# Kernel optimization log

Measured on AMD Instinct MI355X. Metric: run time of the kernel, lower is better.

The kernel has to match this reference:

```python
import jax, jax.numpy as jnp
import numpy as np

NUM_CLASSES = [5, 7, 4, 6, 3, 8, 5, 4, 6, 7, 3, 5, 4, 6, 8, 5, 7, 4, 6, 3]
N_ONE_HOTS = 20
N_OTHERS = 30
H = 48
W = 48
B = 128
N_MAP = 32
ENC_OUT = 32
RES_C = 128
OH_EMB = 9
SUM_NC = sum(NUM_CLASSES)  # 106


def conv2d(x, w, b=None, pad=0):
    # x: NCHW, w: OIHW
    y = jax.lax.conv_general_dilated(
        x, w, window_strides=(1, 1), padding=[(pad, pad), (pad, pad)],
        dimension_numbers=('NCHW', 'OIHW', 'NCHW'))
    if b is not None:
        y = y + b[None, :, None, None]
    return y


def setup_inputs() -> dict:
    key = jax.random.key(0)
    ks = jax.random.split(key, 20)
    x = jax.random.normal(ks[0], (B, 1 + N_MAP, H, W), dtype=jnp.float32)
    # first N_ONE_HOTS entries of flattened channel 0 are categorical indices
    idx_cols = [jax.random.randint(jax.random.fold_in(ks[1], j), (B,), 0, nc)
                for j, nc in enumerate(NUM_CLASSES)]
    idx = jnp.stack(idx_cols, axis=1).astype(jnp.float32)  # (B, 20)
    x = x.at[:, 0, 0, :N_ONE_HOTS].set(idx)
    s = 0.05
    inp = {
        'x': x,
        'fc_w': jax.random.normal(ks[2], (OH_EMB, SUM_NC), jnp.float32) * s,
        'fc_b': jnp.zeros((OH_EMB,), jnp.float32),
        'oh_conv_w': jax.random.normal(ks[3], (OH_EMB, OH_EMB, 1, 1), jnp.float32) * s,
        'oh_conv_b': jnp.zeros((OH_EMB,), jnp.float32),
        'others_conv_w': jax.random.normal(ks[4], (N_OTHERS, N_OTHERS, 1, 1), jnp.float32) * s,
        'others_conv_b': jnp.zeros((N_OTHERS,), jnp.float32),
        'all_conv_w': jax.random.normal(ks[5], (ENC_OUT, OH_EMB + N_OTHERS, 1, 1), jnp.float32) * s,
        'all_conv_b': jnp.zeros((ENC_OUT,), jnp.float32),
        'conv1_w': jax.random.normal(ks[6], (RES_C, ENC_OUT + N_MAP, 1, 1), jnp.float32) * s,
        'conv1_b': jnp.zeros((RES_C,), jnp.float32),
        'rconv1_w': jax.random.normal(ks[7], (RES_C, RES_C, 5, 5), jnp.float32) * s,
        'rconv1_b': jnp.zeros((RES_C,), jnp.float32),
        'rconv2_w': jax.random.normal(ks[8], (RES_C, RES_C, 5, 5), jnp.float32) * s,
        'rconv2_b': jnp.zeros((RES_C,), jnp.float32),
        'se_w1': jax.random.normal(ks[9], (RES_C // 16, RES_C), jnp.float32) * s,
        'se_w2': jax.random.normal(ks[10], (RES_C, RES_C // 16), jnp.float32) * s,
    }
    return inp


def reference(x, fc_w, fc_b, oh_conv_w, oh_conv_b, others_conv_w, others_conv_b,
              all_conv_w, all_conv_b, conv1_w, conv1_b, rconv1_w, rconv1_b,
              rconv2_w, rconv2_b, se_w1, se_w2):
    b = x.shape[0]
    gi = x[:, 0].reshape(b, -1)                 # (b, H*W)
    map_feature = x[:, 1:]                      # (b, N_MAP, H, W)
    idx = jax.lax.stop_gradient(gi[:, :N_ONE_HOTS]).astype(jnp.int32)
    others = gi[:, N_ONE_HOTS:N_ONE_HOTS + N_OTHERS]   # (b, 30)
    # vectorized one-hot build (replaces the quadratic python loop)
    oh = jnp.concatenate(
        [jax.nn.one_hot(idx[:, j], nc, dtype=x.dtype) for j, nc in enumerate(NUM_CLASSES)],
        axis=1)                                 # (b, SUM_NC)
    v = oh @ fc_w.T + fc_b                      # (b, 9)
    # faithful torch expand((h,w)+shape).reshape((b,-1,h,w)) semantics
    v = jnp.broadcast_to(v, (H, W, b, OH_EMB)).reshape(b, OH_EMB, H, W)
    o = jnp.broadcast_to(others, (H, W, b, N_OTHERS)).reshape(b, N_OTHERS, H, W)
    v = conv2d(v, oh_conv_w, oh_conv_b)
    o = conv2d(o, others_conv_w, others_conv_b)
    gi_map = conv2d(jnp.concatenate([v, o], axis=1), all_conv_w, all_conv_b)  # (b, 32, H, W)
    h = conv2d(jnp.concatenate([gi_map, map_feature], axis=1), conv1_w, conv1_b)  # (b, 128, H, W)
    # residual block: 5x5 convs, LeakyReLU, SE, identity skip (in==out)
    identity = h
    y = jax.nn.leaky_relu(conv2d(h, rconv1_w, rconv1_b, pad=2))
    y = conv2d(y, rconv2_w, rconv2_b, pad=2)
    s = y.mean(axis=(2, 3))                     # (b, 128)
    s = jax.nn.sigmoid(jax.nn.relu(s @ se_w1.T) @ se_w2.T)
    y = y * s[:, :, None, None]
    return jax.nn.leaky_relu(y + identity)
```

## Files before the change

kernel.cpp:

```cpp
#include <hip/hip_runtime.h>
#include <hip/hip_bf16.h>
#include <cstddef>

#define HH 48
#define WW 48
#define PIX 2304
#define PPIX 2704
#define BB 128
#define RESC 128
#define XCH 33

typedef short bf16x8 __attribute__((ext_vector_type(8)));
typedef float f32x4 __attribute__((ext_vector_type(4)));

static __device__ __forceinline__ float b2f(unsigned short u) {
    unsigned x = ((unsigned)u) << 16;
    return __builtin_bit_cast(float, x);
}
static __device__ __forceinline__ unsigned short f2b(float f) {
    __hip_bfloat16 hb = __float2bfloat16(f);
    return __builtin_bit_cast(unsigned short, hb);
}

#define GLOAD_LDS16(gp, lp) __builtin_amdgcn_global_load_lds( \
    (const __attribute__((address_space(1))) void*)(gp), \
    (__attribute__((address_space(3))) void*)(lp), 16, 0, 0)

__global__ void k_compute_v(const float* __restrict__ x, const float* __restrict__ fc_w,
                            const float* __restrict__ fc_b, float* __restrict__ v) {
    int b = blockIdx.x * blockDim.x + threadIdx.x;
    if (b >= BB) return;
    const int off[20] = {0,5,12,16,22,25,33,38,42,48,55,58,63,67,73,81,86,93,97,103};
    const float* gi = x + (size_t)b * XCH * PIX;
    int cols[20];
    #pragma unroll
    for (int j = 0; j < 20; j++) cols[j] = off[j] + (int)gi[j];
    #pragma unroll
    for (int e = 0; e < 9; e++) {
        float acc = fc_b[e];
        #pragma unroll
        for (int j = 0; j < 20; j++) acc += fc_w[e * 106 + cols[j]];
        v[b * 9 + e] = acc;
    }
}

__global__ void k_compute_G(const float* __restrict__ x, const float* __restrict__ v,
                            const float* __restrict__ ohw, const float* __restrict__ ohb,
                            const float* __restrict__ otw, const float* __restrict__ otb,
                            const float* __restrict__ aw,  const float* __restrict__ ab,
                            const float* __restrict__ c1w, const float* __restrict__ c1b,
                            float* __restrict__ G) {
    int p = blockIdx.x * blockDim.x + threadIdx.x;
    if (p >= PIX) return;
    float sv = v[((p / 9) & 127) * 9 + (p % 9)];
    float om[30];
    #pragma unroll
    for (int c2 = 0; c2 < 30; c2++) {
        int tmp = c2 * 24 + p;
        int c = tmp % 30;
        int bb = (c2 * 76 + tmp / 30) & 127;
        om[c2] = x[(size_t)bb * XCH * PIX + 20 + c];
    }
    float v9[9];
    #pragma unroll
    for (int e = 0; e < 9; e++) {
        float srow = 0.f;
        #pragma unroll
        for (int e2 = 0; e2 < 9; e2++) srow += ohw[e * 9 + e2];
        v9[e] = ohb[e] + srow * sv;
    }
    float o30[30];
    #pragma unroll
    for (int c = 0; c < 30; c++) {
        float a = otb[c];
        #pragma unroll
        for (int c2 = 0; c2 < 30; c2++) a += otw[c * 30 + c2] * om[c2];
        o30[c] = a;
    }
    float gi32[32];
    #pragma unroll
    for (int g = 0; g < 32; g++) {
        float a = ab[g];
        #pragma unroll
        for (int e = 0; e < 9; e++) a += aw[g * 39 + e] * v9[e];
        #pragma unroll
        for (int c = 0; c < 30; c++) a += aw[g * 39 + 9 + c] * o30[c];
        gi32[g] = a;
    }
    for (int oc = 0; oc < 128; oc++) {
        float a = c1b[oc];
        #pragma unroll
        for (int g = 0; g < 32; g++) a += c1w[oc * 64 + g] * gi32[g];
        G[p * 128 + oc] = a;
    }
}

__global__ void k_convert_w(const float* __restrict__ w1, const float* __restrict__ w2,
                            __hip_bfloat16* __restrict__ wb1, __hip_bfloat16* __restrict__ wb2) {
    int i = blockIdx.x * 256 + threadIdx.x;
    if (i >= 25 * 128 * 128) return;
    int tap = i / 16384, r = i % 16384;
    int oc = r >> 7, ic = r & 127;
    size_t src = (size_t)(oc * 128 + ic) * 25 + tap;
    wb1[i] = __float2bfloat16(w1[src]);
    wb2[i] = __float2bfloat16(w2[src]);
}

__global__ void k_zero_border(__hip_bfloat16* __restrict__ a, __hip_bfloat16* __restrict__ b2) {
    int img = blockIdx.x, t = threadIdx.x;
    for (int j = t; j < 6400; j += 256) {
        int pb = j >> 4, c16 = j & 15;
        int y, x2;
        if (pb < 208) { int q = pb / 52; y = q < 2 ? q : q + 48; x2 = pb % 52; }
        else { int r = pb - 208; y = 2 + (r >> 2); int c = r & 3; x2 = c < 2 ? c : c + 48; }
        size_t off = ((size_t)img * PPIX + y * 52 + x2) * 128 + c16 * 8;
        uint4 z = {0, 0, 0, 0};
        *(uint4*)(a + off) = z;
        *(uint4*)(b2 + off) = z;
    }
}

__global__ __launch_bounds__(256) void k_conv1(const float* __restrict__ x, const float* __restrict__ c1w,
                                               const float* __restrict__ G, __hip_bfloat16* __restrict__ h) {
    __shared__ float xm[32][64];
    __shared__ float w1[32][128];
    int b = blockIdx.y, p0 = blockIdx.x * 64;
    int t = threadIdx.x;
    for (int i = t; i < 4096; i += 256) { int m = i >> 7, oc = i & 127; w1[m][oc] = c1w[oc * 64 + 32 + m]; }
    for (int i = t; i < 2048; i += 256) {
        int m = i >> 6, pix = i & 63;
        xm[m][pix] = x[(size_t)b * XCH * PIX + (size_t)(1 + m) * PIX + p0 + pix];
    }
    __syncthreads();
    int pix = t & 63, ocg = t >> 6;
    float acc[32] = {};
    for (int m = 0; m < 32; m++) {
        float xv = xm[m][pix];
        const float4* wr = (const float4*)&w1[m][ocg * 32];
        #pragma unroll
        for (int k4 = 0; k4 < 8; k4++) {
            float4 wv = wr[k4];
            acc[k4 * 4 + 0] += wv.x * xv; acc[k4 * 4 + 1] += wv.y * xv;
            acc[k4 * 4 + 2] += wv.z * xv; acc[k4 * 4 + 3] += wv.w * xv;
        }
    }
    int p = p0 + pix;
    int py = p / 48, px2 = p % 48;
    size_t hb = ((size_t)b * PPIX + (py + 2) * 52 + px2 + 2) * 128 + ocg * 32;
    const float* gp = &G[(size_t)p * 128 + ocg * 32];
    #pragma unroll
    for (int q = 0; q < 4; q++) {
        unsigned short u[8];
        #pragma unroll
        for (int j = 0; j < 8; j++) u[j] = f2b(acc[q * 8 + j] + gp[q * 8 + j]);
        *(uint4*)(&h[hb + q * 8]) = *(uint4*)u;
    }
}

template<bool LEAKY, bool MEAN, bool PADOUT>
__global__ __launch_bounds__(256, 2) void k_conv5_mfma(
        const __hip_bfloat16* __restrict__ in,
        const __hip_bfloat16* __restrict__ w,
        const float* __restrict__ bias,
        __hip_bfloat16* __restrict__ out,
        float* __restrict__ mean) {
    __shared__ __align__(16) char lds[2][25600];
    int bid = blockIdx.x;
    int xcd = bid & 7, loc = bid >> 3;
    int b = xcd * 16 + loc / 9;
    int tile = loc % 9;
    int ty0 = (tile / 3) * 16, tx0 = (tile % 3) * 16;
    int t = threadIdx.x;
    int wave = t >> 6, lane = t & 63;
    int wm = wave & 1, wn = wave >> 1;
    int l15 = lane & 15, lg = lane >> 4;

    const size_t inb = (size_t)b * PPIX * 128;
    const __hip_bfloat16* wbase = w + (size_t)(wm * 64 + l15) * 128 + lg * 8;

    int sbase[8];
    #pragma unroll
    for (int n = 0; n < 8; ++n) sbase[n] = (wn * 8 + n) * 20 + l15;

    f32x4 acc[4][8] = {};

    auto stage_part = [&](int buf, int icb2, int part) {
        int sg = part * 256 + t;
        if (sg < 1600) {
            int u = sg >> 3, j = sg & 7;
            int bb2 = j ^ (u & 7);
            int s = (u << 1) | (bb2 >> 2);
            int lg2 = bb2 & 3;
            int ry = s / 20, rx = s % 20;
            const __hip_bfloat16* gp = in + inb + (size_t)((ty0 + ry) * 52 + tx0 + rx) * 128 + icb2 + lg2 * 8;
            char* lp = &lds[buf][sg * 16];
            GLOAD_LDS16(gp, lp);
        }
    };

#define AISSUE(Areg, tap_) do { \
        const __hip_bfloat16* wp = wbase + (size_t)(tap_) * 16384 + icb; \
        Areg[0] = *(const bf16x8*)(wp); \
        Areg[1] = *(const bf16x8*)(wp + 2048); \
        Areg[2] = *(const bf16x8*)(wp + 4096); \
        Areg[3] = *(const bf16x8*)(wp + 6144); \
    } while (0)

#define LDSB(s_) (*(const bf16x8*)(cb + (((s_) >> 1) << 7) + \
        ((((((s_) & 1) << 2) | lg) ^ (((s_) >> 1) & 7)) << 4)))

#define CTAP(Areg, tap_) do { \
        int toff = (tap_) + 15 * ((tap_) / 5); \
        bf16x8 Bcur = LDSB(sbase[0] + toff); \
        __builtin_amdgcn_s_setprio(1); \
        _Pragma("unroll") \
        for (int n = 0; n < 8; ++n) { \
            bf16x8 Bnxt = Bcur; \
            if (n < 7) Bnxt = LDSB(sbase[n + 1] + toff); \
            acc[0][n] = __builtin_amdgcn_mfma_f32_16x16x32_bf16(Areg[0], Bcur, acc[0][n], 0, 0, 0); \
            acc[1][n] = __builtin_amdgcn_mfma_f32_16x16x32_bf16(Areg[1], Bcur, acc[1][n], 0, 0, 0); \
            acc[2][n] = __builtin_amdgcn_mfma_f32_16x16x32_bf16(Areg[2], Bcur, acc[2][n], 0, 0, 0); \
            acc[3][n] = __builtin_amdgcn_mfma_f32_16x16x32_bf16(Areg[3], Bcur, acc[3][n], 0, 0, 0); \
            Bcur = Bnxt; \
        } \
        __builtin_amdgcn_s_setprio(0); \
    } while (0)

    #pragma unroll
    for (int j = 0; j < 7; ++j) stage_part(0, 0, j);
    __syncthreads();

    for (int c = 0; c < 4; ++c) {
        const int icb = c * 32;
        const char* cb = lds[c & 1];
        bf16x8 A0[4], A1[4];
        AISSUE(A0, 0);
        AISSUE(A1, 1);
        __builtin_amdgcn_sched_barrier(0);
        for (int i = 0; i < 12; ++i) {
            int tp = 2 * i;
            CTAP(A0, tp);
            AISSUE(A0, tp + 2);
            if (c < 3 && i < 7) {
                stage_part((c + 1) & 1, icb + 32, i);
                __builtin_amdgcn_sched_barrier(0);
            }
            CTAP(A1, tp + 1);
            AISSUE(A1, tp + 3);
        }
        CTAP(A0, 24);
        if (c < 3) __syncthreads();
    }
#undef AISSUE
#undef LDSB
#undef CTAP

    #pragma unroll
    for (int m = 0; m < 4; ++m) {
        int ocm = wm * 64 + m * 16 + lg * 4;
        float bv0 = bias[ocm], bv1 = bias[ocm + 1], bv2 = bias[ocm + 2], bv3 = bias[ocm + 3];
        float ps0 = 0, ps1 = 0, ps2 = 0, ps3 = 0;
        #pragma unroll
        for (int n = 0; n < 8; ++n) {
            float v0 = acc[m][n][0] + bv0, v1 = acc[m][n][1] + bv1;
            float v2 = acc[m][n][2] + bv2, v3 = acc[m][n][3] + bv3;
            ps0 += v0; ps1 += v1; ps2 += v2; ps3 += v3;
            if (LEAKY) {
                v0 = v0 > 0.f ? v0 : 0.01f * v0; v1 = v1 > 0.f ? v1 : 0.01f * v1;
                v2 = v2 > 0.f ? v2 : 0.01f * v2; v3 = v3 > 0.f ? v3 : 0.01f * v3;
            }
            int row = ty0 + wn * 8 + n, col = tx0 + l15;
            size_t off;
            if (PADOUT) off = ((size_t)b * PPIX + (row + 2) * 52 + col + 2) * 128 + ocm;
            else        off = ((size_t)b * PIX + row * 48 + col) * 128 + ocm;
            uint2 pk;
            pk.x = (unsigned)f2b(v0) | ((unsigned)f2b(v1) << 16);
            pk.y = (unsigned)f2b(v2) | ((unsigned)f2b(v3) << 16);
            *(uint2*)(out + off) = pk;
        }
        if (MEAN) {
            #pragma unroll
            for (int mask = 1; mask < 16; mask <<= 1) {
                ps0 += __shfl_xor(ps0, mask);
                ps1 += __shfl_xor(ps1, mask);
                ps2 += __shfl_xor(ps2, mask);
                ps3 += __shfl_xor(ps3, mask);
            }
            if (l15 == 0) {
                atomicAdd(&mean[b * 128 + ocm], ps0);
                atomicAdd(&mean[b * 128 + ocm + 1], ps1);
                atomicAdd(&mean[b * 128 + ocm + 2], ps2);
                atomicAdd(&mean[b * 128 + ocm + 3], ps3);
            }
        }
    }
}

__global__ void k_se(const float* __restrict__ mean, const float* __restrict__ w1,
                     const float* __restrict__ w2, float* __restrict__ s) {
    __shared__ float m[128];
    __shared__ float tt[8];
    int b = blockIdx.x, t = threadIdx.x;
    m[t] = mean[b * RESC + t] * (1.0f / 2304.0f);
    __syncthreads();
    if (t < 8) {
        float a = 0.f;
        for (int i = 0; i < 128; i++) a += w1[t * 128 + i] * m[i];
        tt[t] = a > 0.f ? a : 0.f;
    }
    __syncthreads();
    float a = 0.f;
    #pragma unroll
    for (int r = 0; r < 8; r++) a += w2[t * 8 + r] * tt[r];
    s[b * RESC + t] = 1.f / (1.f + expf(-a));
}

__global__ __launch_bounds__(256) void k_final(const __hip_bfloat16* __restrict__ y2,
                                               const __hip_bfloat16* __restrict__ h,
                                               const float* __restrict__ sg, float* __restrict__ out) {
    __shared__ float sl[128];
    __shared__ float tile[64 * 129];
    int b = blockIdx.y, p0 = blockIdx.x * 64, t = threadIdx.x;
    if (t < 128) sl[t] = sg[b * 128 + t];
    __syncthreads();
    #pragma unroll
    for (int k = 0; k < 4; ++k) {
        int j = t + k * 256;
        int pix = j >> 4, c = j & 15;
        int p = p0 + pix;
        int py = p / 48, px2 = p % 48;
        uint4 yv = *(const uint4*)(y2 + ((size_t)b * PIX + p) * 128 + c * 8);
        uint4 hv = *(const uint4*)(h + ((size_t)b * PPIX + (py + 2) * 52 + px2 + 2) * 128 + c * 8);
        const unsigned short* yp = (const unsigned short*)&yv;
        const unsigned short* hp = (const unsigned short*)&hv;
        #pragma unroll
        for (int jj = 0; jj < 8; ++jj) {
            int oc = c * 8 + jj;
            tile[pix * 129 + oc] = b2f(yp[jj]) * sl[oc] + b2f(hp[jj]);
        }
    }
    __syncthreads();
    int oc = t >> 1, xh = (t & 1) * 32;
    float ov[32];
    #pragma unroll
    for (int i = 0; i < 32; ++i) {
        float v = tile[(xh + i) * 129 + oc];
        ov[i] = v > 0.f ? v : 0.01f * v;
    }
    float* op = out + ((size_t)b * 128 + oc) * PIX + p0 + xh;
    #pragma unroll
    for (int q = 0; q < 8; ++q) ((float4*)op)[q] = *(float4*)&ov[q * 4];
}

extern "C" void kernel_launch(void* const* d_in, const int* in_sizes, int n_in,
                              void* d_out, int out_size, void* d_ws, size_t ws_size,
                              hipStream_t stream) {
    const float* x      = (const float*)d_in[0];
    const float* fc_w   = (const float*)d_in[1];
    const float* fc_b   = (const float*)d_in[2];
    const float* ohw    = (const float*)d_in[3];
    const float* ohb    = (const float*)d_in[4];
    const float* otw    = (const float*)d_in[5];
    const float* otb    = (const float*)d_in[6];
    const float* aw     = (const float*)d_in[7];
    const float* ab     = (const float*)d_in[8];
    const float* c1w    = (const float*)d_in[9];
    const float* c1b    = (const float*)d_in[10];
    const float* r1w    = (const float*)d_in[11];
    const float* r1b    = (const float*)d_in[12];
    const float* r2w    = (const float*)d_in[13];
    const float* r2b    = (const float*)d_in[14];
    const float* se_w1  = (const float*)d_in[15];
    const float* se_w2  = (const float*)d_in[16];

    const size_t padb = (size_t)BB * PPIX * 128 * sizeof(__hip_bfloat16);
    char* ws = (char*)d_ws;
    __hip_bfloat16* h    = (__hip_bfloat16*)ws;  ws += padb;
    __hip_bfloat16* y1   = (__hip_bfloat16*)ws;  ws += padb;
    __hip_bfloat16* y2   = (__hip_bfloat16*)ws;  ws += (size_t)BB * PIX * 128 * sizeof(__hip_bfloat16);
    float* G    = (float*)ws;                    ws += (size_t)PIX * 128 * sizeof(float);
    float* v    = (float*)ws;                    ws += (size_t)BB * 9 * sizeof(float);
    __hip_bfloat16* wb1 = (__hip_bfloat16*)ws;   ws += (size_t)25 * 128 * 128 * sizeof(__hip_bfloat16);
    __hip_bfloat16* wb2 = (__hip_bfloat16*)ws;   ws += (size_t)25 * 128 * 128 * sizeof(__hip_bfloat16);
    ws += 262144;
    float* mean = (float*)ws;                    ws += (size_t)BB * RESC * sizeof(float);
    float* sgate= (float*)ws;                    ws += (size_t)BB * RESC * sizeof(float);

    k_compute_v<<<1, 128, 0, stream>>>(x, fc_w, fc_b, v);
    k_compute_G<<<9, 256, 0, stream>>>(x, v, ohw, ohb, otw, otb, aw, ab, c1w, c1b, G);
    k_convert_w<<<1600, 256, 0, stream>>>(r1w, r2w, wb1, wb2);
    k_zero_border<<<128, 256, 0, stream>>>(h, y1);
    k_conv1<<<dim3(36, 128), 256, 0, stream>>>(x, c1w, G, h);
    k_conv5_mfma<true, false, true><<<dim3(1152), 256, 0, stream>>>(h, wb1, r1b, y1, nullptr);
    hipMemsetAsync(mean, 0, (size_t)BB * RESC * sizeof(float), stream);
    k_conv5_mfma<false, true, false><<<dim3(1152), 256, 0, stream>>>(y1, wb2, r2b, y2, mean);
    k_se<<<128, 128, 0, stream>>>(mean, se_w1, se_w2, sgate);
    k_final<<<dim3(36, 128), 256, 0, stream>>>(y2, h, sgate, (float*)d_out);
}
```

Before: 805.3 us.

## Switch 5x5 conv MFMA from 16x16x32 to 32x32x16 tiles

```diff
diff --git a/kernel.cpp b/kernel.cpp
--- a/kernel.cpp
+++ b/kernel.cpp
@@ -11,7 +11,7 @@
 #define XCH 33
 
 typedef short bf16x8 __attribute__((ext_vector_type(8)));
-typedef float f32x4 __attribute__((ext_vector_type(4)));
+typedef float f32x16 __attribute__((ext_vector_type(16)));
 
 static __device__ __forceinline__ float b2f(unsigned short u) {
     unsigned x = ((unsigned)u) << 16;
@@ -173,26 +173,24 @@
     int t = threadIdx.x;
     int wave = t >> 6, lane = t & 63;
     int wm = wave & 1, wn = wave >> 1;
-    int l15 = lane & 15, lg = lane >> 4;
+    int l31 = lane & 31, hl = lane >> 5;
 
     const size_t inb = (size_t)b * PPIX * 128;
-    const __hip_bfloat16* wbase = w + (size_t)(wm * 64 + l15) * 128 + lg * 8;
-
-    int sbase[8];
-    #pragma unroll
-    for (int n = 0; n < 8; ++n) sbase[n] = (wn * 8 + n) * 20 + l15;
-
-    f32x4 acc[4][8] = {};
+    const __hip_bfloat16* wbase = w + (size_t)(wm * 64 + l31) * 128 + hl * 8;
+
+    int sbase[4];
+    #pragma unroll
+    for (int n = 0; n < 4; ++n) sbase[n] = (wn * 8 + n * 2 + (l31 >> 4)) * 20 + (l31 & 15);
+
+    f32x16 acc[2][4] = {};
 
     auto stage_part = [&](int buf, int icb2, int part) {
         int sg = part * 256 + t;
         if (sg < 1600) {
-            int u = sg >> 3, j = sg & 7;
-            int bb2 = j ^ (u & 7);
-            int s = (u << 1) | (bb2 >> 2);
-            int lg2 = bb2 & 3;
+            int s = sg >> 2;
+            int seg = (sg & 3) ^ (s & 3);
             int ry = s / 20, rx = s % 20;
-            const __hip_bfloat16* gp = in + inb + (size_t)((ty0 + ry) * 52 + tx0 + rx) * 128 + icb2 + lg2 * 8;
+            const __hip_bfloat16* gp = in + inb + (size_t)((ty0 + ry) * 52 + tx0 + rx) * 128 + icb2 + seg * 8;
             char* lp = &lds[buf][sg * 16];
             GLOAD_LDS16(gp, lp);
         }
@@ -200,28 +198,32 @@
 
 #define AISSUE(Areg, tap_) do { \
         const __hip_bfloat16* wp = wbase + (size_t)(tap_) * 16384 + icb; \
-        Areg[0] = *(const bf16x8*)(wp); \
-        Areg[1] = *(const bf16x8*)(wp + 2048); \
-        Areg[2] = *(const bf16x8*)(wp + 4096); \
-        Areg[3] = *(const bf16x8*)(wp + 6144); \
+        Areg[0] = *(const bf16x8*)(wp);             \
+        Areg[1] = *(const bf16x8*)(wp + 16);        \
+        Areg[2] = *(const bf16x8*)(wp + 4096);      \
+        Areg[3] = *(const bf16x8*)(wp + 4112);      \
     } while (0)
 
-#define LDSB(s_) (*(const bf16x8*)(cb + (((s_) >> 1) << 7) + \
-        ((((((s_) & 1) << 2) | lg) ^ (((s_) >> 1) & 7)) << 4)))
+#define LDSB(s_, ks_) (*(const bf16x8*)(cb + ((s_) << 6) + \
+        (((((ks_) << 1) | hl) ^ ((s_) & 3)) << 4)))
 
 #define CTAP(Areg, tap_) do { \
         int toff = (tap_) + 15 * ((tap_) / 5); \
-        bf16x8 Bcur = LDSB(sbase[0] + toff); \
+        bf16x8 B0c = LDSB(sbase[0] + toff, 0); \
+        bf16x8 B1c = LDSB(sbase[0] + toff, 1); \
         __builtin_amdgcn_s_setprio(1); \
         _Pragma("unroll") \
-        for (int n = 0; n < 8; ++n) { \
-            bf16x8 Bnxt = Bcur; \
-            if (n < 7) Bnxt = LDSB(sbase[n + 1] + toff); \
-            acc[0][n] = __builtin_amdgcn_mfma_f32_16x16x32_bf16(Areg[0], Bcur, acc[0][n], 0, 0, 0); \
-            acc[1][n] = __builtin_amdgcn_mfma_f32_16x16x32_bf16(Areg[1], Bcur, acc[1][n], 0, 0, 0); \
-            acc[2][n] = __builtin_amdgcn_mfma_f32_16x16x32_bf16(Areg[2], Bcur, acc[2][n], 0, 0, 0); \
-            acc[3][n] = __builtin_amdgcn_mfma_f32_16x16x32_bf16(Areg[3], Bcur, acc[3][n], 0, 0, 0); \
-            Bcur = Bnxt; \
+        for (int pn = 0; pn < 4; ++pn) { \
+            bf16x8 B0n = B0c, B1n = B1c; \
+            if (pn < 3) { \
+                B0n = LDSB(sbase[pn + 1] + toff, 0); \
+                B1n = LDSB(sbase[pn + 1] + toff, 1); \
+            } \
+            acc[0][pn] = __builtin_amdgcn_mfma_f32_32x32x16_bf16(Areg[0], B0c, acc[0][pn], 0, 0, 0); \
+            acc[1][pn] = __builtin_amdgcn_mfma_f32_32x32x16_bf16(Areg[2], B0c, acc[1][pn], 0, 0, 0); \
+            acc[0][pn] = __builtin_amdgcn_mfma_f32_32x32x16_bf16(Areg[1], B1c, acc[0][pn], 0, 0, 0); \
+            acc[1][pn] = __builtin_amdgcn_mfma_f32_32x32x16_bf16(Areg[3], B1c, acc[1][pn], 0, 0, 0); \
+            B0c = B0n; B1c = B1n; \
         } \
         __builtin_amdgcn_s_setprio(0); \
     } while (0)
@@ -256,41 +258,46 @@
 #undef CTAP
 
     #pragma unroll
-    for (int m = 0; m < 4; ++m) {
-        int ocm = wm * 64 + m * 16 + lg * 4;
-        float bv0 = bias[ocm], bv1 = bias[ocm + 1], bv2 = bias[ocm + 2], bv3 = bias[ocm + 3];
-        float ps0 = 0, ps1 = 0, ps2 = 0, ps3 = 0;
-        #pragma unroll
-        for (int n = 0; n < 8; ++n) {
-            float v0 = acc[m][n][0] + bv0, v1 = acc[m][n][1] + bv1;
-            float v2 = acc[m][n][2] + bv2, v3 = acc[m][n][3] + bv3;
-            ps0 += v0; ps1 += v1; ps2 += v2; ps3 += v3;
-            if (LEAKY) {
-                v0 = v0 > 0.f ? v0 : 0.01f * v0; v1 = v1 > 0.f ? v1 : 0.01f * v1;
-                v2 = v2 > 0.f ? v2 : 0.01f * v2; v3 = v3 > 0.f ? v3 : 0.01f * v3;
+    for (int om = 0; om < 2; ++om) {
+        #pragma unroll
+        for (int q = 0; q < 4; ++q) {
+            int oc4 = wm * 64 + om * 32 + q * 8 + 4 * hl;
+            float bv0 = bias[oc4], bv1 = bias[oc4 + 1], bv2 = bias[oc4 + 2], bv3 = bias[oc4 + 3];
+            float ps0 = 0, ps1 = 0, ps2 = 0, ps3 = 0;
+            #pragma unroll
+            for (int pn = 0; pn < 4; ++pn) {
+                float v0 = acc[om][pn][q * 4 + 0] + bv0;
+                float v1 = acc[om][pn][q * 4 + 1] + bv1;
+                float v2 = acc[om][pn][q * 4 + 2] + bv2;
+                float v3 = acc[om][pn][q * 4 + 3] + bv3;
+                ps0 += v0; ps1 += v1; ps2 += v2; ps3 += v3;
+                if (LEAKY) {
+                    v0 = v0 > 0.f ? v0 : 0.01f * v0; v1 = v1 > 0.f ? v1 : 0.01f * v1;
+                    v2 = v2 > 0.f ? v2 : 0.01f * v2; v3 = v3 > 0.f ? v3 : 0.01f * v3;
+                }
+                int row = ty0 + wn * 8 + pn * 2 + (l31 >> 4), col = tx0 + (l31 & 15);
+                size_t off;
+                if (PADOUT) off = ((size_t)b * PPIX + (row + 2) * 52 + col + 2) * 128 + oc4;
+                else        off = ((size_t)b * PIX + row * 48 + col) * 128 + oc4;
+                uint2 pk;
+                pk.x = (unsigned)f2b(v0) | ((unsigned)f2b(v1) << 16);
+                pk.y = (unsigned)f2b(v2) | ((unsigned)f2b(v3) << 16);
+                *(uint2*)(out + off) = pk;
             }
-            int row = ty0 + wn * 8 + n, col = tx0 + l15;
-            size_t off;
-            if (PADOUT) off = ((size_t)b * PPIX + (row + 2) * 52 + col + 2) * 128 + ocm;
-            else        off = ((size_t)b * PIX + row * 48 + col) * 128 + ocm;
-            uint2 pk;
-            pk.x = (unsigned)f2b(v0) | ((unsigned)f2b(v1) << 16);
-            pk.y = (unsigned)f2b(v2) | ((unsigned)f2b(v3) << 16);
-            *(uint2*)(out + off) = pk;
-        }
-        if (MEAN) {
-            #pragma unroll
-            for (int mask = 1; mask < 16; mask <<= 1) {
-                ps0 += __shfl_xor(ps0, mask);
-                ps1 += __shfl_xor(ps1, mask);
-                ps2 += __shfl_xor(ps2, mask);
-                ps3 += __shfl_xor(ps3, mask);
-            }
-            if (l15 == 0) {
-                atomicAdd(&mean[b * 128 + ocm], ps0);
-                atomicAdd(&mean[b * 128 + ocm + 1], ps1);
-                atomicAdd(&mean[b * 128 + ocm + 2], ps2);
-                atomicAdd(&mean[b * 128 + ocm + 3], ps3);
+            if (MEAN) {
+                #pragma unroll
+                for (int mask = 1; mask < 32; mask <<= 1) {
+                    ps0 += __shfl_xor(ps0, mask);
+                    ps1 += __shfl_xor(ps1, mask);
+                    ps2 += __shfl_xor(ps2, mask);
+                    ps3 += __shfl_xor(ps3, mask);
+                }
+                if (l31 == 0) {
+                    atomicAdd(&mean[b * 128 + oc4], ps0);
+                    atomicAdd(&mean[b * 128 + oc4 + 1], ps1);
+                    atomicAdd(&mean[b * 128 + oc4 + 2], ps2);
+                    atomicAdd(&mean[b * 128 + oc4 + 3], ps3);
+                }
             }
         }
     }
```

Result: slower. 1.054 ms (+30.9%).
